# Optimization experiments

Hardware: AMD Instinct MI355X
Metric: run time of the kernel (lower is better)

The kernel has to match this reference:

```python
import jax, jax.numpy as jnp
import numpy as np

R_MAX = 5.0
NUM_BASIS = 8
CUTOFF_P = 6
N_LAYERS = 3
C = 64          # hidden_mul / channels of irreps_conv_out (64x0e+64x1o)
Z = 4           # element_number
AVG_DEG = 32.0  # num-neighbor normalization (E/N)
SQRT3 = 1.7320508075688772
SQRT2 = 1.4142135623730951


def _radial_embedding(r):
    # Bessel basis * polynomial cutoff (RadialEdgeEmbedding)
    rs = jnp.maximum(r, 1e-9)
    n = jnp.arange(1, NUM_BASIS + 1, dtype=r.dtype)  # (B,)
    bessel = jnp.sqrt(2.0 / R_MAX) * jnp.sin(n * jnp.pi * rs[:, None] / R_MAX) / rs[:, None]
    x = r / R_MAX
    p = float(CUTOFF_P)
    fc = (1.0
          - (p + 1.0) * (p + 2.0) / 2.0 * x ** CUTOFF_P
          + p * (p + 2.0) * x ** (CUTOFF_P + 1)
          - p * (p + 1.0) / 2.0 * x ** (CUTOFF_P + 2))
    fc = jnp.where(x < 1.0, fc, 0.0)
    return bessel * fc[:, None]  # (E, NUM_BASIS)


def setup_inputs() -> dict:
    key = jax.random.key(0)
    ks = jax.random.split(key, 20)
    N, E, B = 16000, 512000, 16
    atom_type = jax.random.randint(ks[0], (N,), 0, Z)
    # atoms in a 4A box so most edge lengths fall inside r_max=5
    atom_pos = jax.random.uniform(ks[1], (N, 3), dtype=jnp.float32) * 4.0
    edge_src = jax.random.randint(ks[2], (E,), 0, N)
    edge_dst = jax.random.randint(ks[3], (E,), 0, N)
    edge_cell_shift = jnp.zeros((E, 3), jnp.float32)
    cell = jnp.tile(jnp.eye(3, dtype=jnp.float32) * 10.0, (B, 1, 1)) \
        + 0.01 * jax.random.normal(ks[4], (B, 3, 3), jnp.float32)
    image_index = jax.random.randint(ks[5], (N,), 0, B)
    g = lambda k, s, fan: jax.random.normal(k, s, jnp.float32) / np.sqrt(fan)
    return {
        'atom_type': atom_type, 'atom_pos': atom_pos,
        'edge_src': edge_src, 'edge_dst': edge_dst,
        'edge_cell_shift': edge_cell_shift, 'cell': cell, 'image_index': image_index,
        'w_lin_in': g(ks[6], (Z, C), Z),
        'mlp_w1': g(ks[7], (N_LAYERS, NUM_BASIS, 64), NUM_BASIS),
        'mlp_b1': jnp.zeros((N_LAYERS, 64), jnp.float32),
        'mlp_w2': g(ks[8], (N_LAYERS, 64, 5 * C), 64),
        'w_self_s': g(ks[9], (N_LAYERS, C, C), C),
        'w_self_v': g(ks[10], (N_LAYERS, C, C), C),
        'w_gate': g(ks[11], (N_LAYERS, C, C), C),
        'w_lin1': g(ks[12], (C, 16), C),
        'w_lin2': g(ks[13], (16, 1), 16),
    }


def reference(atom_type, atom_pos, edge_src, edge_dst, edge_cell_shift, cell,
              image_index, w_lin_in, mlp_w1, mlp_b1, mlp_w2,
              w_self_s, w_self_v, w_gate, w_lin1, w_lin2):
    N = atom_pos.shape[0]
    # edge vectors with periodic cell shift
    edge_vec = atom_pos[edge_dst] - atom_pos[edge_src]
    edge_vec = edge_vec + jnp.einsum('ni,nij->nj', edge_cell_shift,
                                     cell.reshape(-1, 3, 3)[image_index[edge_src]])
    r = jnp.linalg.norm(edge_vec, axis=1)                      # (E,)
    unit = edge_vec / jnp.maximum(r, 1e-9)[:, None]
    # spherical harmonics lmax=1, component normalization: y0=1 (implicit), y1=sqrt(3)*unit
    y1 = SQRT3 * unit                                           # (E, 3)
    emb = _radial_embedding(r)                                  # (E, NUM_BASIS)

    # one-hot embedding + input linear (one-hot is all 0e -> scalar channels only)
    onehot = jax.nn.one_hot(atom_type, Z, dtype=atom_pos.dtype)
    s = onehot @ w_lin_in                                       # (N, C) l=0 features
    v = jnp.zeros((N, C, 3), atom_pos.dtype)                    # (N, C, 3) l=1 features

    inv_sqrt_deg = 1.0 / np.sqrt(AVG_DEG)
    for L in range(N_LAYERS):
        # radial MLP -> per-edge per-channel tensor-product path weights
        w = jax.nn.silu(emb @ mlp_w1[L] + mlp_b1[L]) @ mlp_w2[L]  # (E, 5C)
        w1, w2, w3, w4, w5 = jnp.split(w, 5, axis=1)              # (E, C) each
        s_src = s[edge_src]                                       # (E, C)
        v_src = v[edge_src]                                       # (E, C, 3)
        vdoty = jnp.einsum('ecx,ex->ec', v_src, y1)
        # CG tensor-product paths (l<=1):
        m_s = w1 * s_src + w2 * vdoty / SQRT3                     # 0x0->0, 1x1->0
        m_v = (w3[:, :, None] * s_src[:, :, None] * y1[:, None, :]      # 0x1->1
               + w4[:, :, None] * v_src                                  # 1x0->1
               + w5[:, :, None] * jnp.cross(v_src, y1[:, None, :]) / SQRT2)  # 1x1->1
        agg_s = jax.ops.segment_sum(m_s, edge_dst, num_segments=N) * inv_sqrt_deg
        agg_v = jax.ops.segment_sum(m_v, edge_dst, num_segments=N) * inv_sqrt_deg
        # gated self-interaction + resnet
        gate = jax.nn.sigmoid(agg_s @ w_gate[L])                  # (N, C)
        s = s + jax.nn.silu(agg_s @ w_self_s[L])
        v = v + jnp.einsum('ncx,cd->ndx', agg_v, w_self_v[L]) * gate[:, :, None]

    # o3.Linear to 16x0e then 1x0e (only scalar channels map to 0e outputs)
    atomic_energy = (s @ w_lin1) @ w_lin2                         # (N, 1)
    atomic_energy = atomic_energy * 1.0                           # atomic_scale
    return atomic_energy
```

## Files before the change

kernel.cpp:

```cpp
#include <hip/hip_runtime.h>
#include <hip/hip_fp16.h>
#include <math.h>

#define NUM_BASIS 8
#define SQRT3 1.7320508075688772f
#define SQRT2 1.4142135623730951f
#define INV_SQRT_DEG 0.17677669529663687f
#define PI_F 3.14159265358979323846f

typedef _Float16 half8 __attribute__((ext_vector_type(8)));
typedef float float4v __attribute__((ext_vector_type(4)));

__device__ __forceinline__ float sigmoidf_(float x) { return 1.0f / (1.0f + __expf(-x)); }
__device__ __forceinline__ float siluf_(float x) { return x * sigmoidf_(x); }

__device__ __forceinline__ void unp2(unsigned u, float& a, float& b) {
    __half2 h = *reinterpret_cast<__half2*>(&u);
    float2 f = __half22float2(h);
    a = f.x; b = f.y;
}
__device__ __forceinline__ unsigned pk2(float a, float b) {
    __half2 h = __floats2half2_rn(a, b);
    return *reinterpret_cast<unsigned*>(&h);
}

__global__ __launch_bounds__(256) void count_deg(
    const int* __restrict__ dst, int* __restrict__ deg, int E)
{
    int base = (blockIdx.x * blockDim.x + threadIdx.x) * 4;
    if (base + 3 < E) {
        int4 d4 = *(const int4*)(dst + base);
        atomicAdd(&deg[d4.x], 1);
        atomicAdd(&deg[d4.y], 1);
        atomicAdd(&deg[d4.z], 1);
        atomicAdd(&deg[d4.w], 1);
    } else {
        for (int e = base; e < E; e++) atomicAdd(&deg[dst[e]], 1);
    }
}

__global__ __launch_bounds__(1024) void scan_deg(
    const int* __restrict__ deg, int* __restrict__ cursor, int N)
{
    __shared__ int wsum[16];
    __shared__ int carry_s, tot_s;
    int tid = threadIdx.x;
    int wid = tid >> 6, lane = tid & 63;
    if (tid == 0) carry_s = 0;
    __syncthreads();
    for (int base = 0; base < N; base += 16384) {
        int i0 = base + tid * 16;
        int v[16];
        int sum = 0;
        #pragma unroll
        for (int k = 0; k < 16; k++) {
            int i = i0 + k;
            v[k] = (i < N) ? deg[i] : 0;
            sum += v[k];
        }
        int incl = sum;
        #pragma unroll
        for (int off = 1; off < 64; off <<= 1) {
            int t = __shfl_up(incl, off);
            if (lane >= off) incl += t;
        }
        if (lane == 63) wsum[wid] = incl;
        __syncthreads();
        if (wid == 0 && lane < 16) {
            int wv = wsum[lane];
            int wincl = wv;
            #pragma unroll
            for (int off = 1; off < 16; off <<= 1) {
                int t = __shfl_up(wincl, off);
                if (lane >= off) wincl += t;
            }
            wsum[lane] = wincl - wv;
            if (lane == 15) tot_s = wincl;
        }
        __syncthreads();
        int carry = carry_s;
        int run = carry + wsum[wid] + incl - sum;
        #pragma unroll
        for (int k = 0; k < 16; k++) {
            int i = i0 + k;
            if (i < N) cursor[i] = run;
            run += v[k];
        }
        __syncthreads();
        if (tid == 0) carry_s = carry + tot_s;
        __syncthreads();
    }
}

__global__ __launch_bounds__(256) void edge_pre_scatter(
    const float* __restrict__ pos, const int* __restrict__ src,
    const int* __restrict__ dst, const float* __restrict__ cs,
    const float* __restrict__ cell, const int* __restrict__ img,
    int* __restrict__ cursor, _Float16* __restrict__ emb,
    uint2* __restrict__ y14, int2* __restrict__ sdp, int E)
{
    int e = blockIdx.x * blockDim.x + threadIdx.x;
    if (e >= E) return;
    int si = src[e], di = dst[e];
    int slot = atomicAdd(&cursor[di], 1);
    sdp[slot] = make_int2(si, di);
    float vx = pos[di*3+0] - pos[si*3+0];
    float vy = pos[di*3+1] - pos[si*3+1];
    float vz = pos[di*3+2] - pos[si*3+2];
    float c0 = cs[(size_t)e*3+0], c1 = cs[(size_t)e*3+1], c2 = cs[(size_t)e*3+2];
    const float* M = cell + (size_t)img[si] * 9;
    vx += c0*M[0] + c1*M[3] + c2*M[6];
    vy += c0*M[1] + c1*M[4] + c2*M[7];
    vz += c0*M[2] + c1*M[5] + c2*M[8];
    float r  = sqrtf(vx*vx + vy*vy + vz*vz);
    float rs = fmaxf(r, 1e-9f);
    float inv = 1.0f / rs;
    uint2 yv;
    yv.x = pk2(SQRT3*vx*inv, SQRT3*vy*inv);
    yv.y = pk2(SQRT3*vz*inv, 0.f);
    y14[slot] = yv;
    float x = r * (1.0f / 5.0f);
    float x2 = x*x, x6 = x2*x2*x2;
    float fc = 1.0f - 28.0f*x6 + 48.0f*x6*x - 21.0f*x6*x2;
    if (x >= 1.0f) fc = 0.0f;
    float pre = sqrtf(2.0f / 5.0f) * inv * fc;
    float t = PI_F * rs * (1.0f / 5.0f);
    half8 ev;
    #pragma unroll
    for (int n = 1; n <= NUM_BASIS; n++)
        ev[n-1] = (_Float16)(pre * __sinf((float)n * t));
    *(half8*)(emb + (size_t)slot*NUM_BASIS) = ev;
}

__global__ __launch_bounds__(256) void prep_weights(
    const float* __restrict__ W2, _Float16* __restrict__ w2f,
    const float* __restrict__ Wg, const float* __restrict__ Ws,
    const float* __restrict__ Wv, _Float16* __restrict__ wgtf,
    const float* __restrict__ Wl1, const float* __restrict__ Wl2,
    float* __restrict__ wl12)
{
    int idx = blockIdx.x * blockDim.x + threadIdx.x;
    if (idx < 64) {
        float a = 0.f;
        #pragma unroll
        for (int j = 0; j < 16; j++) a = fmaf(Wl1[idx*16 + j], Wl2[j], a);
        wl12[idx] = a;
    }
    if (idx < 3 * 20480) {
        int L  = idx / 20480;
        int r  = idx % 20480;
        int cg = r / 5120;
        int r2 = r % 5120;
        int p  = r2 / 1024;
        int r3 = r2 % 1024;
        int kh = r3 / 512;
        int r4 = r3 % 512;
        int lane = r4 / 8;
        int j  = r4 % 8;
        int k = kh*32 + (lane >> 4)*8 + j;
        int n = p*64 + cg*16 + (lane & 15);
        w2f[idx] = (_Float16)W2[(size_t)L*20480 + k*320 + n];
    } else if (idx < 3*20480 + 3*3*4096) {
        int idx2 = idx - 3*20480;
        int L   = idx2 / 12288;
        int rem = idx2 % 12288;
        int mat = rem / 4096;
        int r2  = rem % 4096;
        int cg  = r2 / 1024;
        int r3  = r2 % 1024;
        int kh  = r3 / 512;
        int r4  = r3 % 512;
        int lane = r4 / 8;
        int j   = r4 % 8;
        int k = kh*32 + (lane >> 4)*8 + j;
        int n = cg*16 + (lane & 15);
        const float* src = (mat == 0) ? Wg : (mat == 1) ? Ws : Wv;
        wgtf[idx2] = (_Float16)src[(size_t)L*4096 + k*64 + n];
    }
}

__device__ __forceinline__ void mlp1_afrag(
    const _Float16* __restrict__ emb, const float* __restrict__ W1,
    const float* __restrict__ B1, int eA, int q, half8 afrag[2])
{
    half8 ev = *(const half8*)(emb + (size_t)eA*8);
    float em[8];
    #pragma unroll
    for (int j = 0; j < 8; j++) em[j] = (float)ev[j];
    #pragma unroll
    for (int kh = 0; kh < 2; kh++) {
        int kb = kh*32 + q*8;
        float hv[8];
        float4 b0 = *(const float4*)(B1 + kb);
        float4 b1 = *(const float4*)(B1 + kb + 4);
        hv[0]=b0.x; hv[1]=b0.y; hv[2]=b0.z; hv[3]=b0.w;
        hv[4]=b1.x; hv[5]=b1.y; hv[6]=b1.z; hv[7]=b1.w;
        #pragma unroll
        for (int jj = 0; jj < 8; jj++) {
            float4 wa = *(const float4*)(W1 + jj*64 + kb);
            float4 wb = *(const float4*)(W1 + jj*64 + kb + 4);
            hv[0] = fmaf(em[jj], wa.x, hv[0]);
            hv[1] = fmaf(em[jj], wa.y, hv[1]);
            hv[2] = fmaf(em[jj], wa.z, hv[2]);
            hv[3] = fmaf(em[jj], wa.w, hv[3]);
            hv[4] = fmaf(em[jj], wb.x, hv[4]);
            hv[5] = fmaf(em[jj], wb.y, hv[5]);
            hv[6] = fmaf(em[jj], wb.z, hv[6]);
            hv[7] = fmaf(em[jj], wb.w, hv[7]);
        }
        #pragma unroll
        for (int j = 0; j < 8; j++)
            afrag[kh][j] = (_Float16)siluf_(hv[j]);
    }
}

__global__ __launch_bounds__(256) void edge_msg_mfma_l0(
    const _Float16* __restrict__ emb, const uint2* __restrict__ y14,
    const int2* __restrict__ sdp,
    const int* __restrict__ type, const float* __restrict__ wlin,
    const float* __restrict__ W1, const float* __restrict__ B1,
    const _Float16* __restrict__ w2f,
    float* __restrict__ aggs, float* __restrict__ aggx,
    float* __restrict__ aggy, float* __restrict__ aggz, int E)
{
    __shared__ _Float16 w2s[8192];
    {
        half8* dstv = (half8*)w2s;
        const half8* srcv = (const half8*)w2f;
        #pragma unroll
        for (int k = 0; k < 4; k++) {
            int t  = threadIdx.x + k*256;
            int cg = t >> 8;
            int r  = t & 255;
            int pp = r >> 7;
            int rk = r & 127;
            dstv[t] = srcv[cg*640 + pp*256 + rk];
        }
    }
    __syncthreads();

    int wave  = (blockIdx.x * blockDim.x + threadIdx.x) >> 6;
    int lane  = threadIdx.x & 63;
    int wbase = wave * 16;
    if (wbase >= E) return;
    int q   = lane >> 4;
    int col = lane & 15;

    int eb = wbase + q*4;
    int d[4], tt[4];
    float y1x[4], y1y[4], y1z[4];
    #pragma unroll
    for (int r = 0; r < 4; r++) {
        int2 sv = sdp[eb + r];
        tt[r] = type[sv.x];
        d[r]  = sv.y;
        uint2 yv = y14[eb + r];
        float dummy;
        unp2(yv.x, y1x[r], y1y[r]);
        unp2(yv.y, y1z[r], dummy);
    }

    half8 afrag[2];
    mlp1_afrag(emb, W1, B1, wbase + col, q, afrag);

    int dnq = __shfl_down(d[0], 16);
    int nd3 = (q == 3) ? -1 : dnq;
    int df = d[0], dl = d[3];
    bool U = (df == dl);
    int dlp = __shfl_up(dl, 16);
    bool link = (q > 0) && (dlp == df);

    #pragma unroll
    for (int cg = 0; cg < 4; cg++) {
        float4v a1 = {0,0,0,0}, a3 = {0,0,0,0};
        const _Float16* wbp = w2s + ((size_t)cg*2048) + (size_t)lane*8;
        {
            half8 b10 = *(const half8*)(wbp + 0*512);
            half8 b11 = *(const half8*)(wbp + 1*512);
            half8 b30 = *(const half8*)(wbp + 2*512);
            half8 b31 = *(const half8*)(wbp + 3*512);
            a1 = __builtin_amdgcn_mfma_f32_16x16x32_f16(afrag[0], b10, a1, 0, 0, 0);
            a1 = __builtin_amdgcn_mfma_f32_16x16x32_f16(afrag[1], b11, a1, 0, 0, 0);
            a3 = __builtin_amdgcn_mfma_f32_16x16x32_f16(afrag[0], b30, a3, 0, 0, 0);
            a3 = __builtin_amdgcn_mfma_f32_16x16x32_f16(afrag[1], b31, a3, 0, 0, 0);
        }
        int c = cg*16 + col;

        float ms[4], mx[4], my[4], mz[4];
        #pragma unroll
        for (int r = 0; r < 4; r++) {
            float s = wlin[tt[r]*64 + c];
            float w3s = a3[r] * s;
            ms[r] = a1[r] * s;
            mx[r] = w3s * y1x[r];
            my[r] = w3s * y1y[r];
            mz[r] = w3s * y1z[r];
        }
        #pragma unroll
        for (int r = 1; r < 4; r++) {
            if (d[r] == d[r-1]) {
                ms[r] += ms[r-1]; mx[r] += mx[r-1];
                my[r] += my[r-1]; mz[r] += mz[r-1];
            }
        }
        float Cs = 0.f, Cx = 0.f, Cy = 0.f, Cz = 0.f;
        #pragma unroll
        for (int it = 0; it < 3; it++) {
            float es = ms[3] + (U ? Cs : 0.f);
            float ex = mx[3] + (U ? Cx : 0.f);
            float ey = my[3] + (U ? Cy : 0.f);
            float ez = mz[3] + (U ? Cz : 0.f);
            float ts = __shfl_up(es, 16);
            float tx = __shfl_up(ex, 16);
            float ty = __shfl_up(ey, 16);
            float tz = __shfl_up(ez, 16);
            Cs = link ? ts : 0.f; Cx = link ? tx : 0.f;
            Cy = link ? ty : 0.f; Cz = link ? tz : 0.f;
        }
        bool hr = true;
        #pragma unroll
        for (int r = 0; r < 4; r++) {
            if (r > 0) hr = hr && (d[r] == d[r-1]);
            float fs = ms[r] + (hr ? Cs : 0.f);
            float fx = mx[r] + (hr ? Cx : 0.f);
            float fy = my[r] + (hr ? Cy : 0.f);
            float fz = mz[r] + (hr ? Cz : 0.f);
            int ndx = (r < 3) ? d[r+1] : nd3;
            if (ndx != d[r] && d[r] >= 0) {
                size_t ai = (size_t)d[r]*64 + c;
                atomicAdd(aggs + ai, fs);
                atomicAdd(aggx + ai, fx);
                atomicAdd(aggy + ai, fy);
                atomicAdd(aggz + ai, fz);
            }
        }
    }
}

__global__ __launch_bounds__(256) void edge_msg_mfma(
    const _Float16* __restrict__ emb, const uint2* __restrict__ y14,
    const int2* __restrict__ sdp,
    const uint2* __restrict__ nf,
    const float* __restrict__ W1, const float* __restrict__ B1,
    const _Float16* __restrict__ w2f,
    float* __restrict__ aggs, float* __restrict__ aggx,
    float* __restrict__ aggy, float* __restrict__ aggz, int E)
{
    __shared__ _Float16 w2s[10240];
    int cgh = blockIdx.x & 1;
    {
        half8* dstv = (half8*)w2s;
        const half8* srcv = (const half8*)w2f + (size_t)cgh*1280;
        #pragma unroll
        for (int k = 0; k < 5; k++)
            dstv[threadIdx.x + k*256] = srcv[threadIdx.x + k*256];
    }
    __syncthreads();

    int wave  = ((blockIdx.x >> 1) << 2) + (threadIdx.x >> 6);
    int lane  = threadIdx.x & 63;
    int wbase = wave * 16;
    if (wbase >= E) return;
    int q   = lane >> 4;
    int col = lane & 15;

    int eb = wbase + q*4;
    int d[4], si[4];
    float y1x[4], y1y[4], y1z[4];
    #pragma unroll
    for (int r = 0; r < 4; r++) {
        int2 sv = sdp[eb + r];
        si[r] = sv.x;
        d[r]  = sv.y;
        uint2 yv = y14[eb + r];
        float dummy;
        unp2(yv.x, y1x[r], y1y[r]);
        unp2(yv.y, y1z[r], dummy);
    }

    uint2 pf[4][2];
    #pragma unroll
    for (int r = 0; r < 4; r++) {
        size_t nb = (size_t)si[r] * 64 + cgh*32 + col;
        pf[r][0] = nf[nb];
        pf[r][1] = nf[nb + 16];
    }

    half8 afrag[2];
    mlp1_afrag(emb, W1, B1, wbase + col, q, afrag);

    int dnq = __shfl_down(d[0], 16);
    int nd3 = (q == 3) ? -1 : dnq;
    int df = d[0], dl = d[3];
    bool U = (df == dl);
    int dlp = __shfl_up(dl, 16);
    bool link = (q > 0) && (dlp == df);

    #pragma unroll
    for (int cgl = 0; cgl < 2; cgl++) {
        float4v acc[5];
        #pragma unroll
        for (int p = 0; p < 5; p++) acc[p] = (float4v){0.f, 0.f, 0.f, 0.f};
        const _Float16* wbp = w2s + ((size_t)cgl*5120) + (size_t)lane*8;
        #pragma unroll
        for (int p = 0; p < 5; p++) {
            half8 bf0 = *(const half8*)(wbp + ((size_t)(p*2 + 0))*512);
            half8 bf1 = *(const half8*)(wbp + ((size_t)(p*2 + 1))*512);
            acc[p] = __builtin_amdgcn_mfma_f32_16x16x32_f16(afrag[0], bf0, acc[p], 0, 0, 0);
            acc[p] = __builtin_amdgcn_mfma_f32_16x16x32_f16(afrag[1], bf1, acc[p], 0, 0, 0);
        }
        int c = (cgh*2 + cgl)*16 + col;

        float ms[4], mx[4], my[4], mz[4];
        #pragma unroll
        for (int r = 0; r < 4; r++) {
            float fsx, fvx, fvy, fvz;
            unp2(pf[r][cgl].x, fsx, fvx);
            unp2(pf[r][cgl].y, fvy, fvz);
            float yx = y1x[r], yy = y1y[r], yz = y1z[r];
            float w1 = acc[0][r], w2 = acc[1][r], w3 = acc[2][r];
            float w4 = acc[3][r], w5 = acc[4][r];
            float vdoty = fvx*yx + fvy*yy + fvz*yz;
            ms[r] = w1*fsx + w2*vdoty*(1.0f/SQRT3);
            float cx = fvy*yz - fvz*yy;
            float cy = fvz*yx - fvx*yz;
            float cz = fvx*yy - fvy*yx;
            mx[r] = w3*fsx*yx + w4*fvx + w5*cx*(1.0f/SQRT2);
            my[r] = w3*fsx*yy + w4*fvy + w5*cy*(1.0f/SQRT2);
            mz[r] = w3*fsx*yz + w4*fvz + w5*cz*(1.0f/SQRT2);
        }
        #pragma unroll
        for (int r = 1; r < 4; r++) {
            if (d[r] == d[r-1]) {
                ms[r] += ms[r-1]; mx[r] += mx[r-1];
                my[r] += my[r-1]; mz[r] += mz[r-1];
            }
        }
        float Cs = 0.f, Cx = 0.f, Cy = 0.f, Cz = 0.f;
        #pragma unroll
        for (int it = 0; it < 3; it++) {
            float es = ms[3] + (U ? Cs : 0.f);
            float ex = mx[3] + (U ? Cx : 0.f);
            float ey = my[3] + (U ? Cy : 0.f);
            float ez = mz[3] + (U ? Cz : 0.f);
            float ts = __shfl_up(es, 16);
            float tx = __shfl_up(ex, 16);
            float ty = __shfl_up(ey, 16);
            float tz = __shfl_up(ez, 16);
            Cs = link ? ts : 0.f; Cx = link ? tx : 0.f;
            Cy = link ? ty : 0.f; Cz = link ? tz : 0.f;
        }
        bool hr = true;
        #pragma unroll
        for (int r = 0; r < 4; r++) {
            if (r > 0) hr = hr && (d[r] == d[r-1]);
            float fs = ms[r] + (hr ? Cs : 0.f);
            float fx = mx[r] + (hr ? Cx : 0.f);
            float fy = my[r] + (hr ? Cy : 0.f);
            float fz = mz[r] + (hr ? Cz : 0.f);
            int ndx = (r < 3) ? d[r+1] : nd3;
            if (ndx != d[r] && d[r] >= 0) {
                size_t ai = (size_t)d[r]*64 + c;
                atomicAdd(aggs + ai, fs);
                atomicAdd(aggx + ai, fx);
                atomicAdd(aggy + ai, fy);
                atomicAdd(aggz + ai, fz);
            }
        }
    }
}

__global__ __launch_bounds__(256) void node_update_mfma(
    uint2* __restrict__ nf,
    float* __restrict__ aggs, float* __restrict__ aggx,
    float* __restrict__ aggy, float* __restrict__ aggz,
    const _Float16* __restrict__ wgtf,
    const int* __restrict__ type, const float* __restrict__ wlin,
    const float* __restrict__ wl12,
    float* __restrict__ out, int first, int do_out, int N)
{
    __shared__ _Float16 wgs[12288];
    {
        half8* dstv = (half8*)wgs;
        const half8* srcv = (const half8*)wgtf;
        #pragma unroll
        for (int k = 0; k < 6; k++)
            dstv[threadIdx.x + k*256] = srcv[threadIdx.x + k*256];
    }

    int wave  = (blockIdx.x * blockDim.x + threadIdx.x) >> 6;
    int lane  = threadIdx.x & 63;
    int wbase = wave * 16;
    bool active = wbase < N;
    int q = lane >> 4, col = lane & 15;

    int nodeA = active ? (wbase + col) : 0;
    if (nodeA >= N) nodeA = N - 1;
    size_t nb = (size_t)nodeA * 64 + q * 8;
    half8 af0[2], af1[2], af2[2], af3[2];
    #pragma unroll
    for (int kh = 0; kh < 2; kh++) {
        const float* p0 = aggs + nb + kh*32;
        const float* p1 = aggx + nb + kh*32;
        const float* p2 = aggy + nb + kh*32;
        const float* p3 = aggz + nb + kh*32;
        float4 a0 = *(const float4*)p0, b0 = *(const float4*)(p0+4);
        float4 a1 = *(const float4*)p1, b1 = *(const float4*)(p1+4);
        float4 a2 = *(const float4*)p2, b2 = *(const float4*)(p2+4);
        float4 a3 = *(const float4*)p3, b3 = *(const float4*)(p3+4);
        af0[kh][0]=(_Float16)(a0.x*INV_SQRT_DEG); af0[kh][1]=(_Float16)(a0.y*INV_SQRT_DEG);
        af0[kh][2]=(_Float16)(a0.z*INV_SQRT_DEG); af0[kh][3]=(_Float16)(a0.w*INV_SQRT_DEG);
        af0[kh][4]=(_Float16)(b0.x*INV_SQRT_DEG); af0[kh][5]=(_Float16)(b0.y*INV_SQRT_DEG);
        af0[kh][6]=(_Float16)(b0.z*INV_SQRT_DEG); af0[kh][7]=(_Float16)(b0.w*INV_SQRT_DEG);
        af1[kh][0]=(_Float16)(a1.x*INV_SQRT_DEG); af1[kh][1]=(_Float16)(a1.y*INV_SQRT_DEG);
        af1[kh][2]=(_Float16)(a1.z*INV_SQRT_DEG); af1[kh][3]=(_Float16)(a1.w*INV_SQRT_DEG);
        af1[kh][4]=(_Float16)(b1.x*INV_SQRT_DEG); af1[kh][5]=(_Float16)(b1.y*INV_SQRT_DEG);
        af1[kh][6]=(_Float16)(b1.z*INV_SQRT_DEG); af1[kh][7]=(_Float16)(b1.w*INV_SQRT_DEG);
        af2[kh][0]=(_Float16)(a2.x*INV_SQRT_DEG); af2[kh][1]=(_Float16)(a2.y*INV_SQRT_DEG);
        af2[kh][2]=(_Float16)(a2.z*INV_SQRT_DEG); af2[kh][3]=(_Float16)(a2.w*INV_SQRT_DEG);
        af2[kh][4]=(_Float16)(b2.x*INV_SQRT_DEG); af2[kh][5]=(_Float16)(b2.y*INV_SQRT_DEG);
        af2[kh][6]=(_Float16)(b2.z*INV_SQRT_DEG); af2[kh][7]=(_Float16)(b2.w*INV_SQRT_DEG);
        af3[kh][0]=(_Float16)(a3.x*INV_SQRT_DEG); af3[kh][1]=(_Float16)(a3.y*INV_SQRT_DEG);
        af3[kh][2]=(_Float16)(a3.z*INV_SQRT_DEG); af3[kh][3]=(_Float16)(a3.w*INV_SQRT_DEG);
        af3[kh][4]=(_Float16)(b3.x*INV_SQRT_DEG); af3[kh][5]=(_Float16)(b3.y*INV_SQRT_DEG);
        af3[kh][6]=(_Float16)(b3.z*INV_SQRT_DEG); af3[kh][7]=(_Float16)(b3.w*INV_SQRT_DEG);
    }

    int tt[4];
    #pragma unroll
    for (int r = 0; r < 4; r++) {
        int nd = wbase + q*4 + r;
        tt[r] = type[(active && nd < N) ? nd : 0];
    }

    __syncthreads();

    float epart[4] = {0.f, 0.f, 0.f, 0.f};

    #pragma unroll
    for (int cg = 0; cg < 4; cg++) {
        const _Float16* bp = wgs + (size_t)lane * 8;
        half8 bg0 = *(const half8*)(bp + ((size_t)((0*4 + cg)*2 + 0))*512);
        half8 bg1 = *(const half8*)(bp + ((size_t)((0*4 + cg)*2 + 1))*512);
        half8 bs0 = *(const half8*)(bp + ((size_t)((1*4 + cg)*2 + 0))*512);
        half8 bs1 = *(const half8*)(bp + ((size_t)((1*4 + cg)*2 + 1))*512);
        half8 bv0 = *(const half8*)(bp + ((size_t)((2*4 + cg)*2 + 0))*512);
        half8 bv1 = *(const half8*)(bp + ((size_t)((2*4 + cg)*2 + 1))*512);
        float4v ag = {0,0,0,0}, as = {0,0,0,0};
        float4v ox = {0,0,0,0}, oy = {0,0,0,0}, oz = {0,0,0,0};
        ag = __builtin_amdgcn_mfma_f32_16x16x32_f16(af0[0], bg0, ag, 0, 0, 0);
        ag = __builtin_amdgcn_mfma_f32_16x16x32_f16(af0[1], bg1, ag, 0, 0, 0);
        as = __builtin_amdgcn_mfma_f32_16x16x32_f16(af0[0], bs0, as, 0, 0, 0);
        as = __builtin_amdgcn_mfma_f32_16x16x32_f16(af0[1], bs1, as, 0, 0, 0);
        ox = __builtin_amdgcn_mfma_f32_16x16x32_f16(af1[0], bv0, ox, 0, 0, 0);
        ox = __builtin_amdgcn_mfma_f32_16x16x32_f16(af1[1], bv1, ox, 0, 0, 0);
        oy = __builtin_amdgcn_mfma_f32_16x16x32_f16(af2[0], bv0, oy, 0, 0, 0);
        oy = __builtin_amdgcn_mfma_f32_16x16x32_f16(af2[1], bv1, oy, 0, 0, 0);
        oz = __builtin_amdgcn_mfma_f32_16x16x32_f16(af3[0], bv0, oz, 0, 0, 0);
        oz = __builtin_amdgcn_mfma_f32_16x16x32_f16(af3[1], bv1, oz, 0, 0, 0);

        if (!active) continue;
        int c = cg*16 + col;
        float wlc = wl12[c];
        #pragma unroll
        for (int r = 0; r < 4; r++) {
            int nd = wbase + q*4 + r;
            bool wr = nd < N;
            size_t ni = (size_t)nd*64 + c;
            float sx, vx, vy, vz;
            if (first) {
                sx = wlin[tt[r]*64 + c];
                vx = 0.f; vy = 0.f; vz = 0.f;
            } else {
                uint2 cur = nf[wr ? ni : 0];
                unp2(cur.x, sx, vx);
                unp2(cur.y, vy, vz);
            }
            float gate = sigmoidf_(ag[r]);
            sx += siluf_(as[r]);
            vx += ox[r] * gate;
            vy += oy[r] * gate;
            vz += oz[r] * gate;
            if (wr) {
                uint2 nv;
                nv.x = pk2(sx, vx);
                nv.y = pk2(vy, vz);
                nf[ni] = nv;
                aggs[ni] = 0.f;
                aggx[ni] = 0.f;
                aggy[ni] = 0.f;
                aggz[ni] = 0.f;
                epart[r] = fmaf(sx, wlc, epart[r]);
            }
        }
    }
    if (do_out && active) {
        #pragma unroll
        for (int r = 0; r < 4; r++) {
            float e = epart[r];
            e += __shfl_xor(e, 1);
            e += __shfl_xor(e, 2);
            e += __shfl_xor(e, 4);
            e += __shfl_xor(e, 8);
            int nd = wbase + q*4 + r;
            if (col == 0 && nd < N) out[nd] = e;
        }
    }
}

extern "C" void kernel_launch(void* const* d_in, const int* in_sizes, int n_in,
                              void* d_out, int out_size, void* d_ws, size_t ws_size,
                              hipStream_t stream)
{
    const int*   atom_type = (const int*)  d_in[0];
    const float* pos       = (const float*)d_in[1];
    const int*   src       = (const int*)  d_in[2];
    const int*   dst       = (const int*)  d_in[3];
    const float* cs        = (const float*)d_in[4];
    const float* cell      = (const float*)d_in[5];
    const int*   img       = (const int*)  d_in[6];
    const float* wlin_in   = (const float*)d_in[7];
    const float* mw1       = (const float*)d_in[8];
    const float* mb1       = (const float*)d_in[9];
    const float* mw2       = (const float*)d_in[10];
    const float* wss       = (const float*)d_in[11];
    const float* wsv       = (const float*)d_in[12];
    const float* wg        = (const float*)d_in[13];
    const float* wl1       = (const float*)d_in[14];
    const float* wl2       = (const float*)d_in[15];
    int N = in_sizes[0];
    int E = in_sizes[2];

    char* w = (char*)d_ws;
    _Float16* emb = (_Float16*)w; w += (size_t)E * 8 * sizeof(_Float16);
    uint2*  y14  = (uint2*)w;  w += (size_t)E * sizeof(uint2);
    int2*   sdp  = (int2*)w;   w += (size_t)E * sizeof(int2);
    uint2*  nf   = (uint2*)w;  w += (size_t)N * 64 * sizeof(uint2);
    float*  agg  = (float*)w;  w += (size_t)N * 64 * 4 * sizeof(float);
    _Float16* w2f  = (_Float16*)w; w += (size_t)3 * 20480 * sizeof(_Float16);
    _Float16* wgtf = (_Float16*)w; w += (size_t)3 * 3 * 4096 * sizeof(_Float16);
    float*  wl12 = (float*)w;  w += 64 * sizeof(float);
    int*    deg  = (int*)w;    w += (size_t)N * sizeof(int);
    int*    curs = (int*)w;    w += (size_t)N * sizeof(int);

    size_t NC = (size_t)N * 64;
    float* aggs = agg;
    float* aggx = agg + NC;
    float* aggy = agg + 2*NC;
    float* aggz = agg + 3*NC;

    hipMemsetAsync(deg, 0, (size_t)N * sizeof(int), stream);
    hipMemsetAsync(agg, 0, NC * 4 * sizeof(float), stream);
    count_deg<<<(E/4 + 255) / 256, 256, 0, stream>>>(dst, deg, E);
    scan_deg<<<1, 1024, 0, stream>>>(deg, curs, N);
    int prep_n = 3*20480 + 3*3*4096;
    prep_weights<<<(prep_n + 255) / 256, 256, 0, stream>>>(
        mw2, w2f, wg, wss, wsv, wgtf, wl1, wl2, wl12);
    edge_pre_scatter<<<(E + 255) / 256, 256, 0, stream>>>(
        pos, src, dst, cs, cell, img, curs, emb, y14, sdp, E);

    int eblocks = (E + 63) / 64;
    int nblocks = (N + 63) / 64;

    edge_msg_mfma_l0<<<eblocks, 256, 0, stream>>>(
        emb, y14, sdp, atom_type, wlin_in,
        mw1, mb1, w2f, aggs, aggx, aggy, aggz, E);
    node_update_mfma<<<nblocks, 256, 0, stream>>>(
        nf, aggs, aggx, aggy, aggz, wgtf, atom_type, wlin_in, wl12,
        (float*)d_out, 1, 0, N);

    for (int L = 1; L < 3; L++) {
        edge_msg_mfma<<<eblocks * 2, 256, 0, stream>>>(
            emb, y14, sdp, nf,
            mw1 + L * 8 * 64, mb1 + L * 64, w2f + (size_t)L * 20480,
            aggs, aggx, aggy, aggz, E);
        node_update_mfma<<<nblocks, 256, 0, stream>>>(
            nf, aggs, aggx, aggy, aggz,
            wgtf + (size_t)L * 12288, atom_type, wlin_in, wl12,
            (float*)d_out, 0, (L == 2) ? 1 : 0, N);
    }
}
```

Baseline: 523.2 us.

## Fuse edge messages and node update per destination node, precompute MLP hidden

Restructures each layer into one kernel where a block of 8 waves each owns one destination node. Each wave walks that node's CSR-sorted edges, accumulates messages in registers, then applies the gated self-interaction and writes ping-pong node features. This removes the global float atomics/aggregation buffers, their memset and zeroing, and the separate node-update launches. The first radial MLP layer is precomputed into an E×64 fp16 buffer by extra tail blocks of the previous layer, so it overlaps that layer's work. The prep kernels are merged with the scan, and the 1/sqrt3 and 1/sqrt2 factors are folded into the weights. In exchange it adds a large hA memory stream, and per-node work imbalance from varying degree.

```diff
diff --git a/kernel.cpp b/kernel.cpp
--- a/kernel.cpp
+++ b/kernel.cpp
@@ -39,9 +39,53 @@
     }
 }
 
-__global__ __launch_bounds__(1024) void scan_deg(
-    const int* __restrict__ deg, int* __restrict__ cursor, int N)
-{
+__global__ __launch_bounds__(1024) void scan_prep(
+    const int* __restrict__ deg, int* __restrict__ cursor, int N,
+    const float* __restrict__ W2, _Float16* __restrict__ w2f,
+    const float* __restrict__ Wg, const float* __restrict__ Ws,
+    const float* __restrict__ Wv, float* __restrict__ wT,
+    const float* __restrict__ Wl1, const float* __restrict__ Wl2,
+    float* __restrict__ wl12)
+{
+    if (blockIdx.x != 0) {
+        int idx = ((int)blockIdx.x - 1) * 1024 + (int)threadIdx.x;
+        if (idx < 64) {
+            float a = 0.f;
+            #pragma unroll
+            for (int j = 0; j < 16; j++) a = fmaf(Wl1[idx*16 + j], Wl2[j], a);
+            wl12[idx] = a;
+        }
+        if (idx < 3 * 20480) {
+            int L  = idx / 20480;
+            int r  = idx % 20480;
+            int cg = r / 5120;
+            int r2 = r % 5120;
+            int p  = r2 / 1024;
+            int r3 = r2 % 1024;
+            int kh = r3 / 512;
+            int r4 = r3 % 512;
+            int lane = r4 / 8;
+            int j  = r4 % 8;
+            int k = kh*32 + (lane >> 4)*8 + j;
+            int n = p*64 + cg*16 + (lane & 15);
+            float val = W2[(size_t)L*20480 + k*320 + n];
+            if (p == 1)      val *= 0.5773502691896258f;
+            else if (p == 4) val *= 0.7071067811865476f;
+            w2f[idx] = (_Float16)val;
+        } else if (idx < 3*20480 + 3*3*4096) {
+            int idx2 = idx - 3*20480;
+            int L   = idx2 / 12288;
+            int rem = idx2 % 12288;
+            int mat = rem / 4096;
+            int r2  = rem % 4096;
+            int o   = r2 >> 6;
+            int c   = r2 & 63;
+            const float* src = (mat == 0) ? Wg : (mat == 1) ? Ws : Wv;
+            wT[idx2] = src[(size_t)L*4096 + c*64 + o];
+        }
+        return;
+    }
+
     __shared__ int wsum[16];
     __shared__ int carry_s, tot_s;
     int tid = threadIdx.x;
@@ -97,13 +141,13 @@
     const int* __restrict__ dst, const float* __restrict__ cs,
     const float* __restrict__ cell, const int* __restrict__ img,
     int* __restrict__ cursor, _Float16* __restrict__ emb,
-    uint2* __restrict__ y14, int2* __restrict__ sdp, int E)
+    uint2* __restrict__ y14, int* __restrict__ ssrc, int E)
 {
     int e = blockIdx.x * blockDim.x + threadIdx.x;
     if (e >= E) return;
     int si = src[e], di = dst[e];
     int slot = atomicAdd(&cursor[di], 1);
-    sdp[slot] = make_int2(si, di);
+    ssrc[slot] = si;
     float vx = pos[di*3+0] - pos[si*3+0];
     float vy = pos[di*3+1] - pos[si*3+1];
     float vz = pos[di*3+2] - pos[si*3+2];
@@ -132,479 +176,293 @@
     *(half8*)(emb + (size_t)slot*NUM_BASIS) = ev;
 }
 
-__global__ __launch_bounds__(256) void prep_weights(
-    const float* __restrict__ W2, _Float16* __restrict__ w2f,
-    const float* __restrict__ Wg, const float* __restrict__ Ws,
-    const float* __restrict__ Wv, _Float16* __restrict__ wgtf,
-    const float* __restrict__ Wl1, const float* __restrict__ Wl2,
-    float* __restrict__ wl12)
-{
-    int idx = blockIdx.x * blockDim.x + threadIdx.x;
-    if (idx < 64) {
-        float a = 0.f;
-        #pragma unroll
-        for (int j = 0; j < 16; j++) a = fmaf(Wl1[idx*16 + j], Wl2[j], a);
-        wl12[idx] = a;
-    }
-    if (idx < 3 * 20480) {
-        int L  = idx / 20480;
-        int r  = idx % 20480;
-        int cg = r / 5120;
-        int r2 = r % 5120;
-        int p  = r2 / 1024;
-        int r3 = r2 % 1024;
-        int kh = r3 / 512;
-        int r4 = r3 % 512;
-        int lane = r4 / 8;
-        int j  = r4 % 8;
-        int k = kh*32 + (lane >> 4)*8 + j;
-        int n = p*64 + cg*16 + (lane & 15);
-        w2f[idx] = (_Float16)W2[(size_t)L*20480 + k*320 + n];
-    } else if (idx < 3*20480 + 3*3*4096) {
-        int idx2 = idx - 3*20480;
-        int L   = idx2 / 12288;
-        int rem = idx2 % 12288;
-        int mat = rem / 4096;
-        int r2  = rem % 4096;
-        int cg  = r2 / 1024;
-        int r3  = r2 % 1024;
-        int kh  = r3 / 512;
-        int r4  = r3 % 512;
-        int lane = r4 / 8;
-        int j   = r4 % 8;
-        int k = kh*32 + (lane >> 4)*8 + j;
-        int n = cg*16 + (lane & 15);
-        const float* src = (mat == 0) ? Wg : (mat == 1) ? Ws : Wv;
-        wgtf[idx2] = (_Float16)src[(size_t)L*4096 + k*64 + n];
-    }
-}
-
-__device__ __forceinline__ void mlp1_afrag(
+__device__ __forceinline__ void mlp1_pre_body(
     const _Float16* __restrict__ emb, const float* __restrict__ W1,
-    const float* __restrict__ B1, int eA, int q, half8 afrag[2])
-{
-    half8 ev = *(const half8*)(emb + (size_t)eA*8);
-    float em[8];
+    const float* __restrict__ B1, _Float16* __restrict__ hA, int E,
+    int g, int nthreads)
+{
+    int kb   = (g & 7) * 8;
+    int es   = g >> 3;
+    int estr = nthreads >> 3;
+    float wv[8][8];
     #pragma unroll
-    for (int j = 0; j < 8; j++) em[j] = (float)ev[j];
-    #pragma unroll
-    for (int kh = 0; kh < 2; kh++) {
-        int kb = kh*32 + q*8;
+    for (int jj = 0; jj < 8; jj++) {
+        float4 a = *(const float4*)(W1 + jj*64 + kb);
+        float4 b = *(const float4*)(W1 + jj*64 + kb + 4);
+        wv[jj][0]=a.x; wv[jj][1]=a.y; wv[jj][2]=a.z; wv[jj][3]=a.w;
+        wv[jj][4]=b.x; wv[jj][5]=b.y; wv[jj][6]=b.z; wv[jj][7]=b.w;
+    }
+    float bv[8];
+    {
+        float4 a = *(const float4*)(B1 + kb);
+        float4 b = *(const float4*)(B1 + kb + 4);
+        bv[0]=a.x; bv[1]=a.y; bv[2]=a.z; bv[3]=a.w;
+        bv[4]=b.x; bv[5]=b.y; bv[6]=b.z; bv[7]=b.w;
+    }
+    for (int e = es; e < E; e += estr) {
+        half8 ev = *(const half8*)(emb + (size_t)e*8);
         float hv[8];
-        float4 b0 = *(const float4*)(B1 + kb);
-        float4 b1 = *(const float4*)(B1 + kb + 4);
-        hv[0]=b0.x; hv[1]=b0.y; hv[2]=b0.z; hv[3]=b0.w;
-        hv[4]=b1.x; hv[5]=b1.y; hv[6]=b1.z; hv[7]=b1.w;
+        #pragma unroll
+        for (int j = 0; j < 8; j++) hv[j] = bv[j];
         #pragma unroll
         for (int jj = 0; jj < 8; jj++) {
-            float4 wa = *(const float4*)(W1 + jj*64 + kb);
-            float4 wb = *(const float4*)(W1 + jj*64 + kb + 4);
-            hv[0] = fmaf(em[jj], wa.x, hv[0]);
-            hv[1] = fmaf(em[jj], wa.y, hv[1]);
-            hv[2] = fmaf(em[jj], wa.z, hv[2]);
-            hv[3] = fmaf(em[jj], wa.w, hv[3]);
-            hv[4] = fmaf(em[jj], wb.x, hv[4]);
-            hv[5] = fmaf(em[jj], wb.y, hv[5]);
-            hv[6] = fmaf(em[jj], wb.z, hv[6]);
-            hv[7] = fmaf(em[jj], wb.w, hv[7]);
-        }
-        #pragma unroll
-        for (int j = 0; j < 8; j++)
-            afrag[kh][j] = (_Float16)siluf_(hv[j]);
-    }
-}
-
-__global__ __launch_bounds__(256) void edge_msg_mfma_l0(
-    const _Float16* __restrict__ emb, const uint2* __restrict__ y14,
-    const int2* __restrict__ sdp,
+            float em = (float)ev[jj];
+            #pragma unroll
+            for (int j = 0; j < 8; j++)
+                hv[j] = fmaf(em, wv[jj][j], hv[j]);
+        }
+        half8 out;
+        #pragma unroll
+        for (int j = 0; j < 8; j++) out[j] = (_Float16)siluf_(hv[j]);
+        *(half8*)(hA + (size_t)e*64 + kb) = out;
+    }
+}
+
+__global__ __launch_bounds__(256) void mlp1_pre(
+    const _Float16* __restrict__ emb, const float* __restrict__ W1,
+    const float* __restrict__ B1, _Float16* __restrict__ hA, int E)
+{
+    int g = blockIdx.x * blockDim.x + threadIdx.x;
+    mlp1_pre_body(emb, W1, B1, hA, E, g, gridDim.x * blockDim.x);
+}
+
+template<int MODE>
+__global__ __launch_bounds__(512) void fused_layer(
+    const _Float16* __restrict__ hA, const uint2* __restrict__ y14,
+    const int* __restrict__ ssrc, const int* __restrict__ rowend,
+    const uint2* __restrict__ nf_in, uint2* __restrict__ nf_out,
     const int* __restrict__ type, const float* __restrict__ wlin,
-    const float* __restrict__ W1, const float* __restrict__ B1,
-    const _Float16* __restrict__ w2f,
-    float* __restrict__ aggs, float* __restrict__ aggx,
-    float* __restrict__ aggy, float* __restrict__ aggz, int E)
-{
-    __shared__ _Float16 w2s[8192];
+    const _Float16* __restrict__ w2f_L,
+    const float* __restrict__ wgT, const float* __restrict__ wsT,
+    const float* __restrict__ wvT,
+    const float* __restrict__ wl12, float* __restrict__ out, int N,
+    const _Float16* __restrict__ emb, const float* __restrict__ W1n,
+    const float* __restrict__ B1n, _Float16* __restrict__ hAn, int E,
+    int nb_main)
+{
+    if ((int)blockIdx.x >= nb_main) {
+        int g = ((int)blockIdx.x - nb_main) * 512 + (int)threadIdx.x;
+        mlp1_pre_body(emb, W1n, B1n, hAn, E, g,
+                      ((int)gridDim.x - nb_main) * 512);
+        return;
+    }
+
+    constexpr int WSZ = (MODE == 0) ? 8192 : 20480;
+    __shared__ _Float16 w2s[WSZ];
+    __shared__ float aggl[8][4][64];
     {
         half8* dstv = (half8*)w2s;
-        const half8* srcv = (const half8*)w2f;
-        #pragma unroll
-        for (int k = 0; k < 4; k++) {
-            int t  = threadIdx.x + k*256;
-            int cg = t >> 8;
-            int r  = t & 255;
-            int pp = r >> 7;
-            int rk = r & 127;
-            dstv[t] = srcv[cg*640 + pp*256 + rk];
+        const half8* srcv = (const half8*)w2f_L;
+        if (MODE == 0) {
+            #pragma unroll
+            for (int k = 0; k < 2; k++) {
+                int t  = (int)threadIdx.x + k*512;
+                int cg = t >> 8;
+                int r  = t & 255;
+                int pp = r >> 7;
+                int rk = r & 127;
+                dstv[t] = srcv[cg*640 + pp*256 + rk];
+            }
+        } else {
+            #pragma unroll
+            for (int k = 0; k < 5; k++)
+                dstv[threadIdx.x + k*512] = srcv[threadIdx.x + k*512];
         }
     }
     __syncthreads();
 
-    int wave  = (blockIdx.x * blockDim.x + threadIdx.x) >> 6;
-    int lane  = threadIdx.x & 63;
-    int wbase = wave * 16;
-    if (wbase >= E) return;
-    int q   = lane >> 4;
-    int col = lane & 15;
-
-    int eb = wbase + q*4;
-    int d[4], tt[4];
-    float y1x[4], y1y[4], y1z[4];
-    #pragma unroll
-    for (int r = 0; r < 4; r++) {
-        int2 sv = sdp[eb + r];
-        tt[r] = type[sv.x];
-        d[r]  = sv.y;
-        uint2 yv = y14[eb + r];
-        float dummy;
-        unp2(yv.x, y1x[r], y1y[r]);
-        unp2(yv.y, y1z[r], dummy);
-    }
-
-    half8 afrag[2];
-    mlp1_afrag(emb, W1, B1, wbase + col, q, afrag);
-
-    int dnq = __shfl_down(d[0], 16);
-    int nd3 = (q == 3) ? -1 : dnq;
-    int df = d[0], dl = d[3];
-    bool U = (df == dl);
-    int dlp = __shfl_up(dl, 16);
-    bool link = (q > 0) && (dlp == df);
+    int widx = threadIdx.x >> 6;
+    int lane = threadIdx.x & 63;
+    int q = lane >> 4, col = lane & 15;
+    int n = blockIdx.x * 8 + widx;
+    bool nv = n < N;
+    int nn = nv ? n : 0;
+    int rs = (nn > 0) ? rowend[nn-1] : 0;
+    int re = rowend[nn];
+
+    float fss[4] = {0,0,0,0}, fsx[4] = {0,0,0,0};
+    float fsy[4] = {0,0,0,0}, fsz[4] = {0,0,0,0};
+
+    for (int tb = rs; tb < re; tb += 16) {
+        int eA = tb + col;
+        if (eA >= re) eA = re - 1;
+        const _Float16* hp = hA + (size_t)eA*64 + q*8;
+        half8 af0 = *(const half8*)(hp);
+        half8 af1 = *(const half8*)(hp + 32);
+
+        int si4[4], tt4[4];
+        float valf[4];
+        float y1x[4], y1y[4], y1z[4];
+        #pragma unroll
+        for (int r = 0; r < 4; r++) {
+            int e = tb + q*4 + r;
+            bool v = e < re;
+            valf[r] = v ? 1.f : 0.f;
+            if (!v) e = re - 1;
+            si4[r] = ssrc[e];
+            uint2 yv = y14[e];
+            float du;
+            unp2(yv.x, y1x[r], y1y[r]);
+            unp2(yv.y, y1z[r], du);
+        }
+        uint2 pf[4][2];
+        if (MODE != 0) {
+            #pragma unroll
+            for (int r = 0; r < 4; r++) {
+                size_t nb = (size_t)si4[r]*64 + col;
+                pf[r][0] = nf_in[nb];
+                pf[r][1] = nf_in[nb + 16];
+            }
+        } else {
+            #pragma unroll
+            for (int r = 0; r < 4; r++) tt4[r] = type[si4[r]];
+        }
+
+        #pragma unroll
+        for (int cgh = 0; cgh < 2; cgh++) {
+            if (MODE != 0 && cgh == 1) {
+                #pragma unroll
+                for (int r = 0; r < 4; r++) {
+                    size_t nb = (size_t)si4[r]*64 + 32 + col;
+                    pf[r][0] = nf_in[nb];
+                    pf[r][1] = nf_in[nb + 16];
+                }
+            }
+            #pragma unroll
+            for (int cgl = 0; cgl < 2; cgl++) {
+                int cg = cgh*2 + cgl;
+                int c  = cg*16 + col;
+                float ms[4], mx[4], my[4], mz[4];
+                if (MODE == 0) {
+                    float4v a1 = {0,0,0,0}, a3 = {0,0,0,0};
+                    const _Float16* wbp = w2s + (size_t)cg*2048 + (size_t)lane*8;
+                    half8 b10 = *(const half8*)(wbp + 0*512);
+                    half8 b11 = *(const half8*)(wbp + 1*512);
+                    half8 b30 = *(const half8*)(wbp + 2*512);
+                    half8 b31 = *(const half8*)(wbp + 3*512);
+                    a1 = __builtin_amdgcn_mfma_f32_16x16x32_f16(af0, b10, a1, 0, 0, 0);
+                    a1 = __builtin_amdgcn_mfma_f32_16x16x32_f16(af1, b11, a1, 0, 0, 0);
+                    a3 = __builtin_amdgcn_mfma_f32_16x16x32_f16(af0, b30, a3, 0, 0, 0);
+                    a3 = __builtin_amdgcn_mfma_f32_16x16x32_f16(af1, b31, a3, 0, 0, 0);
+                    #pragma unroll
+                    for (int r = 0; r < 4; r++) {
+                        float s = wlin[tt4[r]*64 + c];
+                        float w3s = a3[r] * s;
+                        ms[r] = a1[r] * s;
+                        mx[r] = w3s * y1x[r];
+                        my[r] = w3s * y1y[r];
+                        mz[r] = w3s * y1z[r];
+                    }
+                } else {
+                    float4v acc[5];
+                    #pragma unroll
+                    for (int p = 0; p < 5; p++) acc[p] = (float4v){0.f,0.f,0.f,0.f};
+                    const _Float16* wbp = w2s + (size_t)cg*5120 + (size_t)lane*8;
+                    #pragma unroll
+                    for (int p = 0; p < 5; p++) {
+                        half8 bf0 = *(const half8*)(wbp + ((size_t)(p*2 + 0))*512);
+                        half8 bf1 = *(const half8*)(wbp + ((size_t)(p*2 + 1))*512);
+                        acc[p] = __builtin_amdgcn_mfma_f32_16x16x32_f16(af0, bf0, acc[p], 0, 0, 0);
+                        acc[p] = __builtin_amdgcn_mfma_f32_16x16x32_f16(af1, bf1, acc[p], 0, 0, 0);
+                    }
+                    #pragma unroll
+                    for (int r = 0; r < 4; r++) {
+                        float fsxv, fvx, fvy, fvz;
+                        unp2(pf[r][cgl].x, fsxv, fvx);
+                        unp2(pf[r][cgl].y, fvy, fvz);
+                        float yx = y1x[r], yy = y1y[r], yz = y1z[r];
+                        float w1 = acc[0][r], w2 = acc[1][r], w3 = acc[2][r];
+                        float w4 = acc[3][r], w5 = acc[4][r];
+                        float vdoty = fvx*yx + fvy*yy + fvz*yz;
+                        ms[r] = fmaf(w1, fsxv, w2*vdoty);
+                        float w3s = w3*fsxv;
+                        float cx = fvy*yz - fvz*yy;
+                        float cy = fvz*yx - fvx*yz;
+                        float cz = fvx*yy - fvy*yx;
+                        mx[r] = fmaf(w3s, yx, fmaf(w4, fvx, w5*cx));
+                        my[r] = fmaf(w3s, yy, fmaf(w4, fvy, w5*cy));
+                        mz[r] = fmaf(w3s, yz, fmaf(w4, fvz, w5*cz));
+                    }
+                }
+                #pragma unroll
+                for (int r = 0; r < 4; r++) {
+                    fss[cg] = fmaf(valf[r], ms[r], fss[cg]);
+                    fsx[cg] = fmaf(valf[r], mx[r], fsx[cg]);
+                    fsy[cg] = fmaf(valf[r], my[r], fsy[cg]);
+                    fsz[cg] = fmaf(valf[r], mz[r], fsz[cg]);
+                }
+            }
+        }
+    }
 
     #pragma unroll
     for (int cg = 0; cg < 4; cg++) {
-        float4v a1 = {0,0,0,0}, a3 = {0,0,0,0};
-        const _Float16* wbp = w2s + ((size_t)cg*2048) + (size_t)lane*8;
-        {
-            half8 b10 = *(const half8*)(wbp + 0*512);
-            half8 b11 = *(const half8*)(wbp + 1*512);
-            half8 b30 = *(const half8*)(wbp + 2*512);
-            half8 b31 = *(const half8*)(wbp + 3*512);
-            a1 = __builtin_amdgcn_mfma_f32_16x16x32_f16(afrag[0], b10, a1, 0, 0, 0);
-            a1 = __builtin_amdgcn_mfma_f32_16x16x32_f16(afrag[1], b11, a1, 0, 0, 0);
-            a3 = __builtin_amdgcn_mfma_f32_16x16x32_f16(afrag[0], b30, a3, 0, 0, 0);
-            a3 = __builtin_amdgcn_mfma_f32_16x16x32_f16(afrag[1], b31, a3, 0, 0, 0);
-        }
-        int c = cg*16 + col;
-
-        float ms[4], mx[4], my[4], mz[4];
-        #pragma unroll
-        for (int r = 0; r < 4; r++) {
-            float s = wlin[tt[r]*64 + c];
-            float w3s = a3[r] * s;
-            ms[r] = a1[r] * s;
-            mx[r] = w3s * y1x[r];
-            my[r] = w3s * y1y[r];
-            mz[r] = w3s * y1z[r];
-        }
-        #pragma unroll
-        for (int r = 1; r < 4; r++) {
-            if (d[r] == d[r-1]) {
-                ms[r] += ms[r-1]; mx[r] += mx[r-1];
-                my[r] += my[r-1]; mz[r] += mz[r-1];
-            }
-        }
-        float Cs = 0.f, Cx = 0.f, Cy = 0.f, Cz = 0.f;
-        #pragma unroll
-        for (int it = 0; it < 3; it++) {
-            float es = ms[3] + (U ? Cs : 0.f);
-            float ex = mx[3] + (U ? Cx : 0.f);
-            float ey = my[3] + (U ? Cy : 0.f);
-            float ez = mz[3] + (U ? Cz : 0.f);
-            float ts = __shfl_up(es, 16);
-            float tx = __shfl_up(ex, 16);
-            float ty = __shfl_up(ey, 16);
-            float tz = __shfl_up(ez, 16);
-            Cs = link ? ts : 0.f; Cx = link ? tx : 0.f;
-            Cy = link ? ty : 0.f; Cz = link ? tz : 0.f;
-        }
-        bool hr = true;
-        #pragma unroll
-        for (int r = 0; r < 4; r++) {
-            if (r > 0) hr = hr && (d[r] == d[r-1]);
-            float fs = ms[r] + (hr ? Cs : 0.f);
-            float fx = mx[r] + (hr ? Cx : 0.f);
-            float fy = my[r] + (hr ? Cy : 0.f);
-            float fz = mz[r] + (hr ? Cz : 0.f);
-            int ndx = (r < 3) ? d[r+1] : nd3;
-            if (ndx != d[r] && d[r] >= 0) {
-                size_t ai = (size_t)d[r]*64 + c;
-                atomicAdd(aggs + ai, fs);
-                atomicAdd(aggx + ai, fx);
-                atomicAdd(aggy + ai, fy);
-                atomicAdd(aggz + ai, fz);
-            }
-        }
-    }
-}
-
-__global__ __launch_bounds__(256) void edge_msg_mfma(
-    const _Float16* __restrict__ emb, const uint2* __restrict__ y14,
-    const int2* __restrict__ sdp,
-    const uint2* __restrict__ nf,
-    const float* __restrict__ W1, const float* __restrict__ B1,
-    const _Float16* __restrict__ w2f,
-    float* __restrict__ aggs, float* __restrict__ aggx,
-    float* __restrict__ aggy, float* __restrict__ aggz, int E)
-{
-    __shared__ _Float16 w2s[10240];
-    int cgh = blockIdx.x & 1;
-    {
-        half8* dstv = (half8*)w2s;
-        const half8* srcv = (const half8*)w2f + (size_t)cgh*1280;
-        #pragma unroll
-        for (int k = 0; k < 5; k++)
-            dstv[threadIdx.x + k*256] = srcv[threadIdx.x + k*256];
-    }
-    __syncthreads();
-
-    int wave  = ((blockIdx.x >> 1) << 2) + (threadIdx.x >> 6);
-    int lane  = threadIdx.x & 63;
-    int wbase = wave * 16;
-    if (wbase >= E) return;
-    int q   = lane >> 4;
-    int col = lane & 15;
-
-    int eb = wbase + q*4;
-    int d[4], si[4];
-    float y1x[4], y1y[4], y1z[4];
+        fss[cg] += __shfl_xor(fss[cg], 16); fss[cg] += __shfl_xor(fss[cg], 32);
+        fsx[cg] += __shfl_xor(fsx[cg], 16); fsx[cg] += __shfl_xor(fsx[cg], 32);
+        fsy[cg] += __shfl_xor(fsy[cg], 16); fsy[cg] += __shfl_xor(fsy[cg], 32);
+        fsz[cg] += __shfl_xor(fsz[cg], 16); fsz[cg] += __shfl_xor(fsz[cg], 32);
+        float pv = (q == 0) ? fss[cg] : (q == 1) ? fsx[cg]
+                 : (q == 2) ? fsy[cg] : fsz[cg];
+        aggl[widx][q][cg*16 + col] = pv * INV_SQRT_DEG;
+    }
+    asm volatile("s_waitcnt lgkmcnt(0)" ::: "memory");
+    __builtin_amdgcn_sched_barrier(0);
+
+    const float* agS = &aggl[widx][0][0];
+    const float* agX = &aggl[widx][1][0];
+    const float* agY = &aggl[widx][2][0];
+    const float* agZ = &aggl[widx][3][0];
+    int l = lane;
+    float gv = 0.f, sv = 0.f, ovx = 0.f, ovy = 0.f, ovz = 0.f;
     #pragma unroll
-    for (int r = 0; r < 4; r++) {
-        int2 sv = sdp[eb + r];
-        si[r] = sv.x;
-        d[r]  = sv.y;
-        uint2 yv = y14[eb + r];
-        float dummy;
-        unp2(yv.x, y1x[r], y1y[r]);
-        unp2(yv.y, y1z[r], dummy);
-    }
-
-    uint2 pf[4][2];
-    #pragma unroll
-    for (int r = 0; r < 4; r++) {
-        size_t nb = (size_t)si[r] * 64 + cgh*32 + col;
-        pf[r][0] = nf[nb];
-        pf[r][1] = nf[nb + 16];
-    }
-
-    half8 afrag[2];
-    mlp1_afrag(emb, W1, B1, wbase + col, q, afrag);
-
-    int dnq = __shfl_down(d[0], 16);
-    int nd3 = (q == 3) ? -1 : dnq;
-    int df = d[0], dl = d[3];
-    bool U = (df == dl);
-    int dlp = __shfl_up(dl, 16);
-    bool link = (q > 0) && (dlp == df);
-
-    #pragma unroll
-    for (int cgl = 0; cgl < 2; cgl++) {
-        float4v acc[5];
-        #pragma unroll
-        for (int p = 0; p < 5; p++) acc[p] = (float4v){0.f, 0.f, 0.f, 0.f};
-        const _Float16* wbp = w2s + ((size_t)cgl*5120) + (size_t)lane*8;
-        #pragma unroll
-        for (int p = 0; p < 5; p++) {
-            half8 bf0 = *(const half8*)(wbp + ((size_t)(p*2 + 0))*512);
-            half8 bf1 = *(const half8*)(wbp + ((size_t)(p*2 + 1))*512);
-            acc[p] = __builtin_amdgcn_mfma_f32_16x16x32_f16(afrag[0], bf0, acc[p], 0, 0, 0);
-            acc[p] = __builtin_amdgcn_mfma_f32_16x16x32_f16(afrag[1], bf1, acc[p], 0, 0, 0);
-        }
-        int c = (cgh*2 + cgl)*16 + col;
-
-        float ms[4], mx[4], my[4], mz[4];
-        #pragma unroll
-        for (int r = 0; r < 4; r++) {
-            float fsx, fvx, fvy, fvz;
-            unp2(pf[r][cgl].x, fsx, fvx);
-            unp2(pf[r][cgl].y, fvy, fvz);
-            float yx = y1x[r], yy = y1y[r], yz = y1z[r];
-            float w1 = acc[0][r], w2 = acc[1][r], w3 = acc[2][r];
-            float w4 = acc[3][r], w5 = acc[4][r];
-            float vdoty = fvx*yx + fvy*yy + fvz*yz;
-            ms[r] = w1*fsx + w2*vdoty*(1.0f/SQRT3);
-            float cx = fvy*yz - fvz*yy;
-            float cy = fvz*yx - fvx*yz;
-            float cz = fvx*yy - fvy*yx;
-            mx[r] = w3*fsx*yx + w4*fvx + w5*cx*(1.0f/SQRT2);
-            my[r] = w3*fsx*yy + w4*fvy + w5*cy*(1.0f/SQRT2);
-            mz[r] = w3*fsx*yz + w4*fvz + w5*cz*(1.0f/SQRT2);
-        }
-        #pragma unroll
-        for (int r = 1; r < 4; r++) {
-            if (d[r] == d[r-1]) {
-                ms[r] += ms[r-1]; mx[r] += mx[r-1];
-                my[r] += my[r-1]; mz[r] += mz[r-1];
-            }
-        }
-        float Cs = 0.f, Cx = 0.f, Cy = 0.f, Cz = 0.f;
-        #pragma unroll
-        for (int it = 0; it < 3; it++) {
-            float es = ms[3] + (U ? Cs : 0.f);
-            float ex = mx[3] + (U ? Cx : 0.f);
-            float ey = my[3] + (U ? Cy : 0.f);
-            float ez = mz[3] + (U ? Cz : 0.f);
-            float ts = __shfl_up(es, 16);
-            float tx = __shfl_up(ex, 16);
-            float ty = __shfl_up(ey, 16);
-            float tz = __shfl_up(ez, 16);
-            Cs = link ? ts : 0.f; Cx = link ? tx : 0.f;
-            Cy = link ? ty : 0.f; Cz = link ? tz : 0.f;
-        }
-        bool hr = true;
-        #pragma unroll
-        for (int r = 0; r < 4; r++) {
-            if (r > 0) hr = hr && (d[r] == d[r-1]);
-            float fs = ms[r] + (hr ? Cs : 0.f);
-            float fx = mx[r] + (hr ? Cx : 0.f);
-            float fy = my[r] + (hr ? Cy : 0.f);
-            float fz = mz[r] + (hr ? Cz : 0.f);
-            int ndx = (r < 3) ? d[r+1] : nd3;
-            if (ndx != d[r] && d[r] >= 0) {
-                size_t ai = (size_t)d[r]*64 + c;
-                atomicAdd(aggs + ai, fs);
-                atomicAdd(aggx + ai, fx);
-                atomicAdd(aggy + ai, fy);
-                atomicAdd(aggz + ai, fz);
-            }
-        }
-    }
-}
-
-__global__ __launch_bounds__(256) void node_update_mfma(
-    uint2* __restrict__ nf,
-    float* __restrict__ aggs, float* __restrict__ aggx,
-    float* __restrict__ aggy, float* __restrict__ aggz,
-    const _Float16* __restrict__ wgtf,
-    const int* __restrict__ type, const float* __restrict__ wlin,
-    const float* __restrict__ wl12,
-    float* __restrict__ out, int first, int do_out, int N)
-{
-    __shared__ _Float16 wgs[12288];
-    {
-        half8* dstv = (half8*)wgs;
-        const half8* srcv = (const half8*)wgtf;
-        #pragma unroll
-        for (int k = 0; k < 6; k++)
-            dstv[threadIdx.x + k*256] = srcv[threadIdx.x + k*256];
-    }
-
-    int wave  = (blockIdx.x * blockDim.x + threadIdx.x) >> 6;
-    int lane  = threadIdx.x & 63;
-    int wbase = wave * 16;
-    bool active = wbase < N;
-    int q = lane >> 4, col = lane & 15;
-
-    int nodeA = active ? (wbase + col) : 0;
-    if (nodeA >= N) nodeA = N - 1;
-    size_t nb = (size_t)nodeA * 64 + q * 8;
-    half8 af0[2], af1[2], af2[2], af3[2];
-    #pragma unroll
-    for (int kh = 0; kh < 2; kh++) {
-        const float* p0 = aggs + nb + kh*32;
-        const float* p1 = aggx + nb + kh*32;
-        const float* p2 = aggy + nb + kh*32;
-        const float* p3 = aggz + nb + kh*32;
-        float4 a0 = *(const float4*)p0, b0 = *(const float4*)(p0+4);
-        float4 a1 = *(const float4*)p1, b1 = *(const float4*)(p1+4);
-        float4 a2 = *(const float4*)p2, b2 = *(const float4*)(p2+4);
-        float4 a3 = *(const float4*)p3, b3 = *(const float4*)(p3+4);
-        af0[kh][0]=(_Float16)(a0.x*INV_SQRT_DEG); af0[kh][1]=(_Float16)(a0.y*INV_SQRT_DEG);
-        af0[kh][2]=(_Float16)(a0.z*INV_SQRT_DEG); af0[kh][3]=(_Float16)(a0.w*INV_SQRT_DEG);
-        af0[kh][4]=(_Float16)(b0.x*INV_SQRT_DEG); af0[kh][5]=(_Float16)(b0.y*INV_SQRT_DEG);
-        af0[kh][6]=(_Float16)(b0.z*INV_SQRT_DEG); af0[kh][7]=(_Float16)(b0.w*INV_SQRT_DEG);
-        af1[kh][0]=(_Float16)(a1.x*INV_SQRT_DEG); af1[kh][1]=(_Float16)(a1.y*INV_SQRT_DEG);
-        af1[kh][2]=(_Float16)(a1.z*INV_SQRT_DEG); af1[kh][3]=(_Float16)(a1.w*INV_SQRT_DEG);
-        af1[kh][4]=(_Float16)(b1.x*INV_SQRT_DEG); af1[kh][5]=(_Float16)(b1.y*INV_SQRT_DEG);
-        af1[kh][6]=(_Float16)(b1.z*INV_SQRT_DEG); af1[kh][7]=(_Float16)(b1.w*INV_SQRT_DEG);
-        af2[kh][0]=(_Float16)(a2.x*INV_SQRT_DEG); af2[kh][1]=(_Float16)(a2.y*INV_SQRT_DEG);
-        af2[kh][2]=(_Float16)(a2.z*INV_SQRT_DEG); af2[kh][3]=(_Float16)(a2.w*INV_SQRT_DEG);
-        af2[kh][4]=(_Float16)(b2.x*INV_SQRT_DEG); af2[kh][5]=(_Float16)(b2.y*INV_SQRT_DEG);
-        af2[kh][6]=(_Float16)(b2.z*INV_SQRT_DEG); af2[kh][7]=(_Float16)(b2.w*INV_SQRT_DEG);
-        af3[kh][0]=(_Float16)(a3.x*INV_SQRT_DEG); af3[kh][1]=(_Float16)(a3.y*INV_SQRT_DEG);
-        af3[kh][2]=(_Float16)(a3.z*INV_SQRT_DEG); af3[kh][3]=(_Float16)(a3.w*INV_SQRT_DEG);
-        af3[kh][4]=(_Float16)(b3.x*INV_SQRT_DEG); af3[kh][5]=(_Float16)(b3.y*INV_SQRT_DEG);
-        af3[kh][6]=(_Float16)(b3.z*INV_SQRT_DEG); af3[kh][7]=(_Float16)(b3.w*INV_SQRT_DEG);
-    }
-
-    int tt[4];
-    #pragma unroll
-    for (int r = 0; r < 4; r++) {
-        int nd = wbase + q*4 + r;
-        tt[r] = type[(active && nd < N) ? nd : 0];
-    }
-
-    __syncthreads();
-
-    float epart[4] = {0.f, 0.f, 0.f, 0.f};
-
-    #pragma unroll
-    for (int cg = 0; cg < 4; cg++) {
-        const _Float16* bp = wgs + (size_t)lane * 8;
-        half8 bg0 = *(const half8*)(bp + ((size_t)((0*4 + cg)*2 + 0))*512);
-        half8 bg1 = *(const half8*)(bp + ((size_t)((0*4 + cg)*2 + 1))*512);
-        half8 bs0 = *(const half8*)(bp + ((size_t)((1*4 + cg)*2 + 0))*512);
-        half8 bs1 = *(const half8*)(bp + ((size_t)((1*4 + cg)*2 + 1))*512);
-        half8 bv0 = *(const half8*)(bp + ((size_t)((2*4 + cg)*2 + 0))*512);
-        half8 bv1 = *(const half8*)(bp + ((size_t)((2*4 + cg)*2 + 1))*512);
-        float4v ag = {0,0,0,0}, as = {0,0,0,0};
-        float4v ox = {0,0,0,0}, oy = {0,0,0,0}, oz = {0,0,0,0};
-        ag = __builtin_amdgcn_mfma_f32_16x16x32_f16(af0[0], bg0, ag, 0, 0, 0);
-        ag = __builtin_amdgcn_mfma_f32_16x16x32_f16(af0[1], bg1, ag, 0, 0, 0);
-        as = __builtin_amdgcn_mfma_f32_16x16x32_f16(af0[0], bs0, as, 0, 0, 0);
-        as = __builtin_amdgcn_mfma_f32_16x16x32_f16(af0[1], bs1, as, 0, 0, 0);
-        ox = __builtin_amdgcn_mfma_f32_16x16x32_f16(af1[0], bv0, ox, 0, 0, 0);
-        ox = __builtin_amdgcn_mfma_f32_16x16x32_f16(af1[1], bv1, ox, 0, 0, 0);
-        oy = __builtin_amdgcn_mfma_f32_16x16x32_f16(af2[0], bv0, oy, 0, 0, 0);
-        oy = __builtin_amdgcn_mfma_f32_16x16x32_f16(af2[1], bv1, oy, 0, 0, 0);
-        oz = __builtin_amdgcn_mfma_f32_16x16x32_f16(af3[0], bv0, oz, 0, 0, 0);
-        oz = __builtin_amdgcn_mfma_f32_16x16x32_f16(af3[1], bv1, oz, 0, 0, 0);
-
-        if (!active) continue;
-        int c = cg*16 + col;
-        float wlc = wl12[c];
-        #pragma unroll
-        for (int r = 0; r < 4; r++) {
-            int nd = wbase + q*4 + r;
-            bool wr = nd < N;
-            size_t ni = (size_t)nd*64 + c;
-            float sx, vx, vy, vz;
-            if (first) {
-                sx = wlin[tt[r]*64 + c];
-                vx = 0.f; vy = 0.f; vz = 0.f;
-            } else {
-                uint2 cur = nf[wr ? ni : 0];
-                unp2(cur.x, sx, vx);
-                unp2(cur.y, vy, vz);
-            }
-            float gate = sigmoidf_(ag[r]);
-            sx += siluf_(as[r]);
-            vx += ox[r] * gate;
-            vy += oy[r] * gate;
-            vz += oz[r] * gate;
-            if (wr) {
-                uint2 nv;
-                nv.x = pk2(sx, vx);
-                nv.y = pk2(vy, vz);
-                nf[ni] = nv;
-                aggs[ni] = 0.f;
-                aggx[ni] = 0.f;
-                aggy[ni] = 0.f;
-                aggz[ni] = 0.f;
-                epart[r] = fmaf(sx, wlc, epart[r]);
-            }
-        }
-    }
-    if (do_out && active) {
-        #pragma unroll
-        for (int r = 0; r < 4; r++) {
-            float e = epart[r];
-            e += __shfl_xor(e, 1);
-            e += __shfl_xor(e, 2);
-            e += __shfl_xor(e, 4);
-            e += __shfl_xor(e, 8);
-            int nd = wbase + q*4 + r;
-            if (col == 0 && nd < N) out[nd] = e;
-        }
+    for (int cc = 0; cc < 64; cc += 4) {
+        float4 aS = *(const float4*)(agS + cc);
+        float4 aX = *(const float4*)(agX + cc);
+        float4 aY = *(const float4*)(agY + cc);
+        float4 aZ = *(const float4*)(agZ + cc);
+        float4 g4 = *(const float4*)(wgT + (size_t)l*64 + cc);
+        float4 s4 = *(const float4*)(wsT + (size_t)l*64 + cc);
+        float4 v4 = *(const float4*)(wvT + (size_t)l*64 + cc);
+        gv = fmaf(aS.x, g4.x, gv); gv = fmaf(aS.y, g4.y, gv);
+        gv = fmaf(aS.z, g4.z, gv); gv = fmaf(aS.w, g4.w, gv);
+        sv = fmaf(aS.x, s4.x, sv); sv = fmaf(aS.y, s4.y, sv);
+        sv = fmaf(aS.z, s4.z, sv); sv = fmaf(aS.w, s4.w, sv);
+        ovx = fmaf(aX.x, v4.x, ovx); ovx = fmaf(aX.y, v4.y, ovx);
+        ovx = fmaf(aX.z, v4.z, ovx); ovx = fmaf(aX.w, v4.w, ovx);
+        ovy = fmaf(aY.x, v4.x, ovy); ovy = fmaf(aY.y, v4.y, ovy);
+        ovy = fmaf(aY.z, v4.z, ovy); ovy = fmaf(aY.w, v4.w, ovy);
+        ovz = fmaf(aZ.x, v4.x, ovz); ovz = fmaf(aZ.y, v4.y, ovz);
+        ovz = fmaf(aZ.z, v4.z, ovz); ovz = fmaf(aZ.w, v4.w, ovz);
+    }
+
+    float sxo, vxo, vyo, vzo;
+    if (MODE == 0) {
+        sxo = wlin[type[nn]*64 + l];
+        vxo = 0.f; vyo = 0.f; vzo = 0.f;
+    } else {
+        uint2 cur = nf_in[(size_t)nn*64 + l];
+        unp2(cur.x, sxo, vxo);
+        unp2(cur.y, vyo, vzo);
+    }
+    float gate = sigmoidf_(gv);
+    sxo += siluf_(sv);
+    vxo = fmaf(ovx, gate, vxo);
+    vyo = fmaf(ovy, gate, vyo);
+    vzo = fmaf(ovz, gate, vzo);
+
+    if (MODE != 2) {
+        if (nv) {
+            uint2 nvv;
+            nvv.x = pk2(sxo, vxo);
+            nvv.y = pk2(vyo, vzo);
+            nf_out[(size_t)nn*64 + l] = nvv;
+        }
+    } else {
+        float e = sxo * wl12[l];
+        e += __shfl_xor(e, 1);  e += __shfl_xor(e, 2);
+        e += __shfl_xor(e, 4);  e += __shfl_xor(e, 8);
+        e += __shfl_xor(e, 16); e += __shfl_xor(e, 32);
+        if (nv && lane == 0) out[nn] = e;
     }
 }
 
@@ -634,49 +492,65 @@
     char* w = (char*)d_ws;
     _Float16* emb = (_Float16*)w; w += (size_t)E * 8 * sizeof(_Float16);
     uint2*  y14  = (uint2*)w;  w += (size_t)E * sizeof(uint2);
-    int2*   sdp  = (int2*)w;   w += (size_t)E * sizeof(int2);
-    uint2*  nf   = (uint2*)w;  w += (size_t)N * 64 * sizeof(uint2);
-    float*  agg  = (float*)w;  w += (size_t)N * 64 * 4 * sizeof(float);
-    _Float16* w2f  = (_Float16*)w; w += (size_t)3 * 20480 * sizeof(_Float16);
-    _Float16* wgtf = (_Float16*)w; w += (size_t)3 * 3 * 4096 * sizeof(_Float16);
+    int*    ssrc = (int*)w;    w += (size_t)E * sizeof(int);
+    uint2*  nfA  = (uint2*)w;  w += (size_t)N * 64 * sizeof(uint2);
+    uint2*  nfB  = (uint2*)w;  w += (size_t)N * 64 * sizeof(uint2);
+    _Float16* w2f = (_Float16*)w; w += (size_t)3 * 20480 * sizeof(_Float16);
+    float*  wT   = (float*)w;  w += (size_t)3 * 3 * 4096 * sizeof(float);
     float*  wl12 = (float*)w;  w += 64 * sizeof(float);
     int*    deg  = (int*)w;    w += (size_t)N * sizeof(int);
     int*    curs = (int*)w;    w += (size_t)N * sizeof(int);
 
-    size_t NC = (size_t)N * 64;
-    float* aggs = agg;
-    float* aggx = agg + NC;
-    float* aggy = agg + 2*NC;
-    float* aggz = agg + 3*NC;
+    size_t used   = (size_t)(w - (char*)d_ws);
+    size_t hbytes = (size_t)E * 64 * sizeof(_Float16);
+    _Float16* hA0 = (_Float16*)w;
+    bool two_h = (ws_size >= used + 2*hbytes);
+    _Float16* hA1 = two_h ? (_Float16*)(w + hbytes) : hA0;
 
     hipMemsetAsync(deg, 0, (size_t)N * sizeof(int), stream);
-    hipMemsetAsync(agg, 0, NC * 4 * sizeof(float), stream);
     count_deg<<<(E/4 + 255) / 256, 256, 0, stream>>>(dst, deg, E);
-    scan_deg<<<1, 1024, 0, stream>>>(deg, curs, N);
     int prep_n = 3*20480 + 3*3*4096;
-    prep_weights<<<(prep_n + 255) / 256, 256, 0, stream>>>(
-        mw2, w2f, wg, wss, wsv, wgtf, wl1, wl2, wl12);
+    scan_prep<<<1 + (prep_n + 1023) / 1024, 1024, 0, stream>>>(
+        deg, curs, N, mw2, w2f, wg, wss, wsv, wT, wl1, wl2, wl12);
     edge_pre_scatter<<<(E + 255) / 256, 256, 0, stream>>>(
-        pos, src, dst, cs, cell, img, curs, emb, y14, sdp, E);
-
-    int eblocks = (E + 63) / 64;
-    int nblocks = (N + 63) / 64;
-
-    edge_msg_mfma_l0<<<eblocks, 256, 0, stream>>>(
-        emb, y14, sdp, atom_type, wlin_in,
-        mw1, mb1, w2f, aggs, aggx, aggy, aggz, E);
-    node_update_mfma<<<nblocks, 256, 0, stream>>>(
-        nf, aggs, aggx, aggy, aggz, wgtf, atom_type, wlin_in, wl12,
-        (float*)d_out, 1, 0, N);
-
-    for (int L = 1; L < 3; L++) {
-        edge_msg_mfma<<<eblocks * 2, 256, 0, stream>>>(
-            emb, y14, sdp, nf,
-            mw1 + L * 8 * 64, mb1 + L * 64, w2f + (size_t)L * 20480,
-            aggs, aggx, aggy, aggz, E);
-        node_update_mfma<<<nblocks, 256, 0, stream>>>(
-            nf, aggs, aggx, aggy, aggz,
-            wgtf + (size_t)L * 12288, atom_type, wlin_in, wl12,
-            (float*)d_out, 0, (L == 2) ? 1 : 0, N);
-    }
-}
+        pos, src, dst, cs, cell, img, curs, emb, y14, ssrc, E);
+
+    int nbm  = (N + 7) / 8;
+    int tail = 1024;
+
+    const float* wT0 = wT;
+    const float* wT1 = wT + 12288;
+    const float* wT2 = wT + 24576;
+
+    mlp1_pre<<<2048, 256, 0, stream>>>(emb, mw1, mb1, hA0, E);
+
+    if (two_h) {
+        fused_layer<0><<<nbm + tail, 512, 0, stream>>>(
+            hA0, y14, ssrc, curs, nfB, nfA, atom_type, wlin_in,
+            w2f, wT0, wT0 + 4096, wT0 + 8192, wl12, (float*)d_out, N,
+            emb, mw1 + 512, mb1 + 64, hA1, E, nbm);
+        fused_layer<1><<<nbm + tail, 512, 0, stream>>>(
+            hA1, y14, ssrc, curs, nfA, nfB, atom_type, wlin_in,
+            w2f + 20480, wT1, wT1 + 4096, wT1 + 8192, wl12, (float*)d_out, N,
+            emb, mw1 + 1024, mb1 + 128, hA0, E, nbm);
+        fused_layer<2><<<nbm, 512, 0, stream>>>(
+            hA0, y14, ssrc, curs, nfB, nfA, atom_type, wlin_in,
+            w2f + 40960, wT2, wT2 + 4096, wT2 + 8192, wl12, (float*)d_out, N,
+            emb, mw1, mb1, hA0, E, nbm);
+    } else {
+        fused_layer<0><<<nbm, 512, 0, stream>>>(
+            hA0, y14, ssrc, curs, nfB, nfA, atom_type, wlin_in,
+            w2f, wT0, wT0 + 4096, wT0 + 8192, wl12, (float*)d_out, N,
+            emb, mw1, mb1, hA0, E, nbm);
+        mlp1_pre<<<2048, 256, 0, stream>>>(emb, mw1 + 512, mb1 + 64, hA0, E);
+        fused_layer<1><<<nbm, 512, 0, stream>>>(
+            hA0, y14, ssrc, curs, nfA, nfB, atom_type, wlin_in,
+            w2f + 20480, wT1, wT1 + 4096, wT1 + 8192, wl12, (float*)d_out, N,
+            emb, mw1, mb1, hA0, E, nbm);
+        mlp1_pre<<<2048, 256, 0, stream>>>(emb, mw1 + 1024, mb1 + 128, hA0, E);
+        fused_layer<2><<<nbm, 512, 0, stream>>>(
+            hA0, y14, ssrc, curs, nfB, nfA, atom_type, wlin_in,
+            w2f + 40960, wT2, wT2 + 4096, wT2 + 8192, wl12, (float*)d_out, N,
+            emb, mw1, mb1, hA0, E, nbm);
+    }
+}
```

Measured after the change: 962.9 us. 84.0% more time.
